# Performance work log

Measured on AMD Instinct MI355X. Metric: run time of the kernel, lower is better.

The kernel has to match this reference:

```python
import jax, jax.numpy as jnp
import numpy as np

DIM = 384
HEADS = 12
WH, WW = 7, 7
SH, SW = 3, 3
MLP_HIDDEN = int(DIM * 4.0)
EPS = 1e-5


def _rel_pos_index(wh, ww):
    coords = np.stack(np.meshgrid(np.arange(wh), np.arange(ww), indexing='ij'))  # (2,wh,ww)
    cf = coords.reshape(2, -1)
    rel = (cf[:, :, None] - cf[:, None, :]).transpose(1, 2, 0).astype(np.int64)  # (N,N,2)
    rel[:, :, 0] += wh - 1
    rel[:, :, 1] += ww - 1
    rel[:, :, 0] *= 2 * ww - 1
    return rel.sum(-1)  # (N,N) indices into (2wh-1)*(2ww-1) table


def _attn_mask(Hp, Wp, wh, ww, sh, sw):
    img = np.zeros((Hp, Wp), dtype=np.float32)
    cnt = 0
    for hsl in (slice(0, -wh), slice(-wh, -sh), slice(-sh, None)):
        for wsl in (slice(0, -ww), slice(-ww, -sw), slice(-sw, None)):
            img[hsl, wsl] = cnt
            cnt += 1
    mw = img.reshape(Hp // wh, wh, Wp // ww, ww).transpose(0, 2, 1, 3).reshape(-1, wh * ww)
    am = mw[:, None, :] - mw[:, :, None]  # (nW,N,N)
    return np.where(am != 0, np.float32(-100.0), np.float32(0.0))


def _ln(x, g, b):
    mu = jnp.mean(x, axis=-1, keepdims=True)
    var = jnp.mean((x - mu) ** 2, axis=-1, keepdims=True)
    return (x - mu) * jax.lax.rsqrt(var + EPS) * g + b


def setup_inputs() -> dict:
    key = jax.random.key(0)
    ks = jax.random.split(key, 12)
    B, H, W, C = 16, 56, 56, DIM
    s = 0.02
    return {
        'x': jax.random.normal(ks[0], (B, H * W, C), jnp.float32),
        'H': H,
        'W': W,
        'norm1_g': jnp.ones((C,), jnp.float32),
        'norm1_b': jnp.zeros((C,), jnp.float32),
        'qkv_w': jax.random.normal(ks[1], (C, 3 * C), jnp.float32) * s,
        'qkv_b': jnp.zeros((3 * C,), jnp.float32),
        'rpb_table': jax.random.normal(ks[2], ((2 * WH - 1) * (2 * WW - 1), HEADS), jnp.float32) * s,
        'proj_w': jax.random.normal(ks[3], (C, C), jnp.float32) * s,
        'proj_b': jnp.zeros((C,), jnp.float32),
        'norm2_g': jnp.ones((C,), jnp.float32),
        'norm2_b': jnp.zeros((C,), jnp.float32),
        'mlp_w1': jax.random.normal(ks[4], (C, MLP_HIDDEN), jnp.float32) * s,
        'mlp_b1': jnp.zeros((MLP_HIDDEN,), jnp.float32),
        'mlp_w2': jax.random.normal(ks[5], (MLP_HIDDEN, C), jnp.float32) * s,
        'mlp_b2': jnp.zeros((C,), jnp.float32),
    }


def reference(x, H, W, norm1_g, norm1_b, qkv_w, qkv_b, rpb_table, proj_w, proj_b,
              norm2_g, norm2_b, mlp_w1, mlp_b1, mlp_w2, mlp_b2):
    B, L, C = x.shape
    hd = C // HEADS
    scale = hd ** (-0.5)
    N = WH * WW

    shortcut = x
    h = _ln(x, norm1_g, norm1_b).reshape(B, H, W, C)

    # pad to window multiple (static python ints)
    pad_b = (WH - H % WH) % WH
    pad_r = (WW - W % WW) % WW
    if pad_b or pad_r:
        h = jnp.pad(h, ((0, 0), (0, pad_b), (0, pad_r), (0, 0)))
    Hp, Wp = H + pad_b, W + pad_r

    # cyclic shift
    if SH or SW:
        h = jnp.roll(h, (-SH, -SW), axis=(1, 2))
        mask = jnp.asarray(_attn_mask(Hp, Wp, WH, WW, SH, SW))  # (nW,N,N)
    else:
        mask = None

    # window partition -> (B*nW, N, C)
    nWh, nWw = Hp // WH, Wp // WW
    nW = nWh * nWw
    hw = h.reshape(B, nWh, WH, nWw, WW, C).transpose(0, 1, 3, 2, 4, 5).reshape(-1, N, C)
    B_ = hw.shape[0]

    # window attention
    qkv = (hw @ qkv_w + qkv_b).reshape(B_, N, 3, HEADS, hd).transpose(2, 0, 3, 1, 4)
    q, k, v = qkv[0], qkv[1], qkv[2]  # (B_, heads, N, hd)
    attn = jnp.einsum('bhnd,bhmd->bhnm', q * scale, k)
    rpi = jnp.asarray(_rel_pos_index(WH, WW))  # (N,N)
    bias = rpb_table[rpi.reshape(-1)].reshape(N, N, HEADS).transpose(2, 0, 1)  # (heads,N,N)
    attn = attn + bias[None]
    if mask is not None:
        attn = attn.reshape(B_ // nW, nW, HEADS, N, N) + mask[None, :, None]
        attn = attn.reshape(-1, HEADS, N, N)
    attn = jax.nn.softmax(attn, axis=-1)
    out = jnp.einsum('bhnm,bhmd->bhnd', attn, v).transpose(0, 2, 1, 3).reshape(B_, N, C)
    out = out @ proj_w + proj_b

    # window reverse
    h = out.reshape(B, nWh, nWw, WH, WW, C).transpose(0, 1, 3, 2, 4, 5).reshape(B, Hp, Wp, C)
    if SH or SW:
        h = jnp.roll(h, (SH, SW), axis=(1, 2))
    if pad_b or pad_r:
        h = h[:, :H, :W, :]
    h = h.reshape(B, H * W, C)

    x = shortcut + h
    m = _ln(x, norm2_g, norm2_b)
    m = jax.nn.gelu(m @ mlp_w1 + mlp_b1, approximate=False) @ mlp_w2 + mlp_b2
    return x + m
```

## Files before the change

### kernel.cpp

```cpp
#include <hip/hip_runtime.h>
#include <cstdint>
#include <cstddef>

typedef __attribute__((ext_vector_type(8))) short short8;
typedef __attribute__((ext_vector_type(4))) float f32x4;
typedef unsigned short u16;

#define CDIM 384

__device__ __forceinline__ u16 f2bf(float f) {
  union { float f; uint32_t u; } v; v.f = f;
  return (u16)((v.u + 0x7FFFu + ((v.u >> 16) & 1u)) >> 16);
}

__device__ __forceinline__ void glds16(const void* g, void* l) {
  __builtin_amdgcn_global_load_lds(
      (__attribute__((address_space(1))) void*)(g),
      (__attribute__((address_space(3))) void*)(l), 16, 0, 0);
}

__global__ void wconv_t(const float* __restrict__ W, u16* __restrict__ Wt, int K, int N) {
  int i = blockIdx.x * 256 + threadIdx.x;
  if (i >= K * N) return;
  int k = i / N, n = i - k * N;
  Wt[(size_t)n * K + k] = f2bf(W[i]);
}

template<bool GATHER>
__global__ __launch_bounds__(256) void ln_kernel(const float* __restrict__ X,
    const float* __restrict__ G, const float* __restrict__ Bp,
    u16* __restrict__ Y) {
  int wid = threadIdx.x >> 6, lane = threadIdx.x & 63;
  int row = blockIdx.x * 4 + wid;
  const float* xr = X + (size_t)row * CDIM;
  float4 a = ((const float4*)xr)[lane];
  float2 b = ((const float2*)xr)[128 + lane];
  float s1 = a.x + a.y + a.z + a.w + b.x + b.y;
  float s2 = a.x*a.x + a.y*a.y + a.z*a.z + a.w*a.w + b.x*b.x + b.y*b.y;
  #pragma unroll
  for (int m = 1; m < 64; m <<= 1) { s1 += __shfl_xor(s1, m, 64); s2 += __shfl_xor(s2, m, 64); }
  float mean = s1 * (1.0f / CDIM);
  float var  = s2 * (1.0f / CDIM) - mean * mean;
  float rstd = rsqrtf(var + 1e-5f);
  float4 g4 = ((const float4*)G)[lane];
  float2 g2 = ((const float2*)G)[128 + lane];
  float4 b4 = ((const float4*)Bp)[lane];
  float2 b2 = ((const float2*)Bp)[128 + lane];
  size_t orow = row;
  if (GATHER) {
    int bb = row / 3136, l = row - bb * 3136;
    int h = l / 56, w = l - h * 56;
    int hs = h - 3; if (hs < 0) hs += 56;
    int wsv = w - 3; if (wsv < 0) wsv += 56;
    int wi = (hs / 7) * 8 + (wsv / 7);
    int n = (hs % 7) * 7 + (wsv % 7);
    orow = (size_t)(bb * 64 + wi) * 49 + n;
  }
  u16* yr = Y + orow * CDIM;
  ushort4 o4;
  o4.x = f2bf((a.x - mean) * rstd * g4.x + b4.x);
  o4.y = f2bf((a.y - mean) * rstd * g4.y + b4.y);
  o4.z = f2bf((a.z - mean) * rstd * g4.z + b4.z);
  o4.w = f2bf((a.w - mean) * rstd * g4.w + b4.w);
  ((ushort4*)yr)[lane] = o4;
  ushort2 o2;
  o2.x = f2bf((b.x - mean) * rstd * g2.x + b2.x);
  o2.y = f2bf((b.y - mean) * rstd * g2.y + b2.y);
  ((ushort2*)yr)[128 + lane] = o2;
}

template<int MODE>
__global__ __launch_bounds__(256) void gemm_bt(
    const u16* __restrict__ A, const u16* __restrict__ Bt,
    const float* __restrict__ bias, const float* __restrict__ extra,
    void* __restrict__ outp, int K) {
  __shared__ __align__(16) u16 As[4096];
  __shared__ __align__(16) u16 Bs[4096];
  int tid = threadIdx.x;
  int lane = tid & 63, wid = tid >> 6;
  int ln = lane & 15, g = lane >> 4;
  int wm = (wid >> 1) * 64, wn = (wid & 1) * 64;
  int bn = blockIdx.x, bm = blockIdx.y;
  int rs = K >> 3;
  const short8* Ag = (const short8*)(A + (size_t)bm * 128 * K);
  const short8* Bg = (const short8*)(Bt + (size_t)bn * 128 * K);
  int c0 = tid, c1 = tid + 256;
  int r0 = c0 >> 2, q0 = c0 & 3, r1 = c1 >> 2, q1 = c1 & 3;
  f32x4 acc[4][4] = {};
  int nk = K >> 5;
  for (int kt = 0; kt < nk; ++kt) {
    int ko = kt * 4;
    glds16(&Ag[r0 * rs + ko + q0], &((short8*)As)[c0]);
    glds16(&Ag[r1 * rs + ko + q1], &((short8*)As)[c1]);
    glds16(&Bg[r0 * rs + ko + q0], &((short8*)Bs)[c0]);
    glds16(&Bg[r1 * rs + ko + q1], &((short8*)Bs)[c1]);
    __syncthreads();
    short8 af[4], bf[4];
    #pragma unroll
    for (int mi = 0; mi < 4; ++mi) af[mi] = ((short8*)As)[(wm + mi * 16 + ln) * 4 + g];
    #pragma unroll
    for (int ni = 0; ni < 4; ++ni) bf[ni] = ((short8*)Bs)[(wn + ni * 16 + ln) * 4 + g];
    #pragma unroll
    for (int mi = 0; mi < 4; ++mi)
      #pragma unroll
      for (int ni = 0; ni < 4; ++ni)
        acc[mi][ni] = __builtin_amdgcn_mfma_f32_16x16x32_bf16(af[mi], bf[ni], acc[mi][ni], 0, 0, 0);
    __syncthreads();
  }
  int Rbase = bm * 128 + wm + g * 4;
  int Cbase = bn * 128 + wn + ln;
  #pragma unroll
  for (int mi = 0; mi < 4; ++mi) {
    #pragma unroll
    for (int r = 0; r < 4; ++r) {
      int R = Rbase + mi * 16 + r;
      #pragma unroll
      for (int ni = 0; ni < 4; ++ni) {
        int Cc = Cbase + ni * 16;
        float v = acc[mi][ni][r] + bias[Cc];
        if (MODE == 0) {
          int w_ = R / 49, n = R - w_ * 49;
          int t = Cc / 384, rem = Cc - t * 384;
          int hh = rem >> 5, d = rem & 31;
          ((u16*)outp)[((size_t)(w_ * 3 + t) * 12 + hh) * 1568 + n * 32 + d] = f2bf(v);
        } else if (MODE == 1) {
          int w_ = R / 49, n = R - w_ * 49;
          int bb = w_ >> 6, wi = w_ & 63;
          int hs = (wi >> 3) * 7 + n / 7;
          int wsv = (wi & 7) * 7 + n % 7;
          int h2 = hs + 3; if (h2 >= 56) h2 -= 56;
          int w2 = wsv + 3; if (w2 >= 56) w2 -= 56;
          size_t idx = ((size_t)bb * 3136 + h2 * 56 + w2) * 384 + Cc;
          ((float*)outp)[idx] = extra[idx] + v;
        } else if (MODE == 2) {
          float gl = 0.5f * v * (1.0f + erff(v * 0.70710678118f));
          ((u16*)outp)[(size_t)R * 1536 + Cc] = f2bf(gl);
        } else {
          size_t idx = (size_t)R * 384 + Cc;
          ((float*)outp)[idx] = extra[idx] + v;
        }
      }
    }
  }
}

__global__ __launch_bounds__(128) void attn_kernel(
    const u16* __restrict__ qkv, const float* __restrict__ rpb,
    u16* __restrict__ aout) {
  __shared__ __align__(16) u16 lds[2][10240];
  int wid = threadIdx.x >> 6, lane = threadIdx.x & 63;
  int task = blockIdx.x * 2 + wid;
  int w_ = task / 12, hh = task - w_ * 12;
  int wi = w_ & 63;
  u16* Q  = lds[wid];
  u16* Kt = Q + 2048;
  u16* Vt = Q + 4096;
  u16* P  = Q + 6144;
  const short8* qb = (const short8*)(qkv + ((size_t)w_ * 36 + hh) * 1568);
  const short8* kb = (const short8*)(qkv + ((size_t)w_ * 36 + 12 + hh) * 1568);
  const short8* vb = (const short8*)(qkv + ((size_t)w_ * 36 + 24 + hh) * 1568);
  short8 zz = {0, 0, 0, 0, 0, 0, 0, 0};
  for (int c = 196 + lane; c < 256; c += 64) { ((short8*)Q)[c] = zz; ((short8*)Kt)[c] = zz; }
  for (int c = lane; c < 256; c += 64) ((short8*)Vt)[c] = zz;
  __syncthreads();
  for (int c = lane; c < 196; c += 64) {
    ((short8*)Q)[c]  = qb[c];
    ((short8*)Kt)[c] = kb[c];
    short8 vv = vb[c];
    int n = c >> 2, d0 = (c & 3) << 3;
    #pragma unroll
    for (int j = 0; j < 8; ++j) Vt[(d0 + j) * 64 + n] = (u16)vv[j];
  }
  __syncthreads();
  int ln = lane & 15, g = lane >> 4;
  short8 ak[4], bq[4];
  #pragma unroll
  for (int mi = 0; mi < 4; ++mi) ak[mi] = ((const short8*)Kt)[(mi * 16 + ln) * 4 + g];
  #pragma unroll
  for (int ni = 0; ni < 4; ++ni) bq[ni] = ((const short8*)Q)[(ni * 16 + ln) * 4 + g];
  f32x4 zf = {0.f, 0.f, 0.f, 0.f};
  f32x4 s[4][4];
  #pragma unroll
  for (int mi = 0; mi < 4; ++mi)
    #pragma unroll
    for (int ni = 0; ni < 4; ++ni)
      s[mi][ni] = __builtin_amdgcn_mfma_f32_16x16x32_bf16(ak[mi], bq[ni], zf, 0, 0, 0);
  const float scale = 0.17677669529663687f;
  int hb = (wi >> 3) * 7, wb = (wi & 7) * 7;
  #pragma unroll
  for (int ni = 0; ni < 4; ++ni) {
    int n = ni * 16 + ln;
    bool nv = n < 49;
    int nh = n / 7, nw = n - nh * 7;
    int hsn = hb + nh, wsn = wb + nw;
    int rn = (hsn < 49 ? 0 : (hsn < 53 ? 1 : 2)) * 3 + (wsn < 49 ? 0 : (wsn < 53 ? 1 : 2));
    float pv[16];
    float mx = -3.0e38f;
    #pragma unroll
    for (int mi = 0; mi < 4; ++mi) {
      #pragma unroll
      for (int r = 0; r < 4; ++r) {
        int m = mi * 16 + g * 4 + r;
        float v = -1.0e9f;
        if (nv && m < 49) {
          int mh = m / 7, mw = m - mh * 7;
          int hsm = hb + mh, wsm = wb + mw;
          int rm = (hsm < 49 ? 0 : (hsm < 53 ? 1 : 2)) * 3 + (wsm < 49 ? 0 : (wsm < 53 ? 1 : 2));
          int rel = (nh - mh + 6) * 13 + (nw - mw + 6);
          v = s[mi][ni][r] * scale + rpb[rel * 12 + hh];
          if (rn != rm) v -= 100.0f;
        }
        pv[mi * 4 + r] = v;
        mx = fmaxf(mx, v);
      }
    }
    mx = fmaxf(mx, __shfl_xor(mx, 16, 64));
    mx = fmaxf(mx, __shfl_xor(mx, 32, 64));
    float sum = 0.f;
    #pragma unroll
    for (int i = 0; i < 16; ++i) { pv[i] = __expf(pv[i] - mx); sum += pv[i]; }
    sum += __shfl_xor(sum, 16, 64);
    sum += __shfl_xor(sum, 32, 64);
    float inv = 1.0f / sum;
    #pragma unroll
    for (int mi = 0; mi < 4; ++mi) {
      ushort4 pk;
      pk.x = f2bf(pv[mi * 4 + 0] * inv);
      pk.y = f2bf(pv[mi * 4 + 1] * inv);
      pk.z = f2bf(pv[mi * 4 + 2] * inv);
      pk.w = f2bf(pv[mi * 4 + 3] * inv);
      *(ushort4*)(P + n * 64 + mi * 16 + g * 4) = pk;
    }
  }
  __syncthreads();
  f32x4 o[2][4] = {};
  #pragma unroll
  for (int kt = 0; kt < 2; ++kt) {
    short8 av[2], bp[4];
    #pragma unroll
    for (int m2 = 0; m2 < 2; ++m2) av[m2] = ((const short8*)Vt)[(m2 * 16 + ln) * 8 + kt * 4 + g];
    #pragma unroll
    for (int ni = 0; ni < 4; ++ni) bp[ni] = ((const short8*)P)[(ni * 16 + ln) * 8 + kt * 4 + g];
    #pragma unroll
    for (int m2 = 0; m2 < 2; ++m2)
      #pragma unroll
      for (int ni = 0; ni < 4; ++ni)
        o[m2][ni] = __builtin_amdgcn_mfma_f32_16x16x32_bf16(av[m2], bp[ni], o[m2][ni], 0, 0, 0);
  }
  #pragma unroll
  for (int m2 = 0; m2 < 2; ++m2)
    #pragma unroll
    for (int ni = 0; ni < 4; ++ni)
      #pragma unroll
      for (int r = 0; r < 4; ++r) {
        int d = m2 * 16 + g * 4 + r;
        int n = ni * 16 + ln;
        if (n < 49)
          aout[((size_t)w_ * 49 + n) * 384 + hh * 32 + d] = f2bf(o[m2][ni][r]);
      }
}

extern "C" void kernel_launch(void* const* d_in, const int* in_sizes, int n_in,
                              void* d_out, int out_size, void* d_ws, size_t ws_size,
                              hipStream_t stream) {
  const float* x     = (const float*)d_in[0];
  const float* n1g   = (const float*)d_in[3];
  const float* n1b   = (const float*)d_in[4];
  const float* qkvw  = (const float*)d_in[5];
  const float* qkvb  = (const float*)d_in[6];
  const float* rpb   = (const float*)d_in[7];
  const float* projw = (const float*)d_in[8];
  const float* projb = (const float*)d_in[9];
  const float* n2g   = (const float*)d_in[10];
  const float* n2b   = (const float*)d_in[11];
  const float* w1    = (const float*)d_in[12];
  const float* b1    = (const float*)d_in[13];
  const float* w2    = (const float*)d_in[14];
  const float* b2    = (const float*)d_in[15];

  char* ws = (char*)d_ws;
  u16* wqT    = (u16*)(ws + 0);
  u16* wpT    = (u16*)(ws + 884736);
  u16* w1T    = (u16*)(ws + 1179648);
  u16* w2T    = (u16*)(ws + 2359296);
  u16* lnbuf  = (u16*)(ws + 3538944);
  u16* qkvB   = (u16*)(ws + 42074112);
  u16* attnO  = (u16*)(ws + 157679616);
  u16* hidden = qkvB;
  float* xres = (float*)d_out;

  wconv_t<<<(442368 + 255) / 256, 256, 0, stream>>>(qkvw, wqT, 384, 1152);
  wconv_t<<<(147456 + 255) / 256, 256, 0, stream>>>(projw, wpT, 384, 384);
  wconv_t<<<(589824 + 255) / 256, 256, 0, stream>>>(w1, w1T, 384, 1536);
  wconv_t<<<(589824 + 255) / 256, 256, 0, stream>>>(w2, w2T, 1536, 384);

  ln_kernel<true><<<12544, 256, 0, stream>>>(x, n1g, n1b, lnbuf);
  gemm_bt<0><<<dim3(9, 392), 256, 0, stream>>>(lnbuf, wqT, qkvb, nullptr, qkvB, 384);
  attn_kernel<<<6144, 128, 0, stream>>>(qkvB, rpb, attnO);
  gemm_bt<1><<<dim3(3, 392), 256, 0, stream>>>(attnO, wpT, projb, x, xres, 384);
  ln_kernel<false><<<12544, 256, 0, stream>>>(xres, n2g, n2b, lnbuf);
  gemm_bt<2><<<dim3(12, 392), 256, 0, stream>>>(lnbuf, w1T, b1, nullptr, hidden, 384);
  gemm_bt<3><<<dim3(3, 392), 256, 0, stream>>>(hidden, w2T, b2, xres, d_out, 1536);
}
```

Before: 688.0 us.

## Double-buffer GEMM LDS tiles and remap workgroups across XCDs

The GEMM now keeps two LDS buffers for the A and B tiles, so the next K-tile is prefetched with global_load_lds while MFMAs run on the current one, with one barrier per iteration. It also remaps the linear workgroup id so that consecutive tiles land on the same XCD, which should improve L2 reuse of shared A/B panels. The cost is double the LDS per block, which may lower occupancy.

```diff
diff --git a/kernel.cpp b/kernel.cpp
--- a/kernel.cpp
+++ b/kernel.cpp
@@ -17,6 +17,13 @@
   __builtin_amdgcn_global_load_lds(
       (__attribute__((address_space(1))) void*)(g),
       (__attribute__((address_space(3))) void*)(l), 16, 0, 0);
+}
+
+__device__ __forceinline__ int xcd_swz(int orig, int nwg) {
+  int q = nwg >> 3, r = nwg & 7;
+  int x = orig & 7, i = orig >> 3;
+  int base = (x < r) ? x * (q + 1) : r * (q + 1) + (x - r) * q;
+  return base + i;
 }
 
 __global__ void wconv_t(const float* __restrict__ W, u16* __restrict__ Wt, int K, int N) {
@@ -74,13 +81,16 @@
     const u16* __restrict__ A, const u16* __restrict__ Bt,
     const float* __restrict__ bias, const float* __restrict__ extra,
     void* __restrict__ outp, int K) {
-  __shared__ __align__(16) u16 As[4096];
-  __shared__ __align__(16) u16 Bs[4096];
+  __shared__ __align__(16) u16 As[2][4096];
+  __shared__ __align__(16) u16 Bs[2][4096];
   int tid = threadIdx.x;
   int lane = tid & 63, wid = tid >> 6;
   int ln = lane & 15, g = lane >> 4;
   int wm = (wid >> 1) * 64, wn = (wid & 1) * 64;
-  int bn = blockIdx.x, bm = blockIdx.y;
+  int gx = gridDim.x;
+  int nwg = gx * gridDim.y;
+  int id = xcd_swz(blockIdx.y * gx + blockIdx.x, nwg);
+  int bn = id % gx, bm = id / gx;
   int rs = K >> 3;
   const short8* Ag = (const short8*)(A + (size_t)bm * 128 * K);
   const short8* Bg = (const short8*)(Bt + (size_t)bn * 128 * K);
@@ -88,24 +98,32 @@
   int r0 = c0 >> 2, q0 = c0 & 3, r1 = c1 >> 2, q1 = c1 & 3;
   f32x4 acc[4][4] = {};
   int nk = K >> 5;
+  glds16(&Ag[r0 * rs + q0], &((short8*)As[0])[c0]);
+  glds16(&Ag[r1 * rs + q1], &((short8*)As[0])[c1]);
+  glds16(&Bg[r0 * rs + q0], &((short8*)Bs[0])[c0]);
+  glds16(&Bg[r1 * rs + q1], &((short8*)Bs[0])[c1]);
+  __syncthreads();
+  int cur = 0;
   for (int kt = 0; kt < nk; ++kt) {
-    int ko = kt * 4;
-    glds16(&Ag[r0 * rs + ko + q0], &((short8*)As)[c0]);
-    glds16(&Ag[r1 * rs + ko + q1], &((short8*)As)[c1]);
-    glds16(&Bg[r0 * rs + ko + q0], &((short8*)Bs)[c0]);
-    glds16(&Bg[r1 * rs + ko + q1], &((short8*)Bs)[c1]);
-    __syncthreads();
+    if (kt + 1 < nk) {
+      int ko = (kt + 1) * 4;
+      glds16(&Ag[r0 * rs + ko + q0], &((short8*)As[cur ^ 1])[c0]);
+      glds16(&Ag[r1 * rs + ko + q1], &((short8*)As[cur ^ 1])[c1]);
+      glds16(&Bg[r0 * rs + ko + q0], &((short8*)Bs[cur ^ 1])[c0]);
+      glds16(&Bg[r1 * rs + ko + q1], &((short8*)Bs[cur ^ 1])[c1]);
+    }
     short8 af[4], bf[4];
     #pragma unroll
-    for (int mi = 0; mi < 4; ++mi) af[mi] = ((short8*)As)[(wm + mi * 16 + ln) * 4 + g];
-    #pragma unroll
-    for (int ni = 0; ni < 4; ++ni) bf[ni] = ((short8*)Bs)[(wn + ni * 16 + ln) * 4 + g];
+    for (int mi = 0; mi < 4; ++mi) af[mi] = ((short8*)As[cur])[(wm + mi * 16 + ln) * 4 + g];
+    #pragma unroll
+    for (int ni = 0; ni < 4; ++ni) bf[ni] = ((short8*)Bs[cur])[(wn + ni * 16 + ln) * 4 + g];
     #pragma unroll
     for (int mi = 0; mi < 4; ++mi)
       #pragma unroll
       for (int ni = 0; ni < 4; ++ni)
         acc[mi][ni] = __builtin_amdgcn_mfma_f32_16x16x32_bf16(af[mi], bf[ni], acc[mi][ni], 0, 0, 0);
     __syncthreads();
+    cur ^= 1;
   }
   int Rbase = bm * 128 + wm + g * 4;
   int Cbase = bn * 128 + wn + ln;
```

Measured after the change: 664.0 us. 3.5% less time.
